# Kernel tuning notes

Measured on AMD Instinct MI355X. Metric: run time of the kernel, lower is better.

## Reference

```python
import jax, jax.numpy as jnp
import numpy as np

B, C_LIDAR, C_CAM = 2, 384, 80
H = W = 180
HW = H * W
HID, NCLS, P, NH, DFF, L, NMS_K = 128, 10, 200, 8, 256, 2, 3


def conv2d(x, w, b):
    y = jax.lax.conv_general_dilated(x, w, (1, 1), 'SAME', dimension_numbers=('NCHW', 'OIHW', 'NCHW'))
    return y + b[None, :, None, None]


def conv1d3(x, w, b):
    y = jax.lax.conv_general_dilated(x, w, (1,), 'SAME', dimension_numbers=('NCH', 'OIH', 'NCH'))
    return y + b[None, :, None]


def layer_norm(x, g, b, eps=1e-5):
    mu = jnp.mean(x, -1, keepdims=True)
    var = jnp.mean((x - mu) ** 2, -1, keepdims=True)
    return (x - mu) * jax.lax.rsqrt(var + eps) * g + b


def mha(q, k, v, wqkv, bqkv, wo, bo):
    Bq, Nq, C = q.shape
    dh = C // NH
    qh = (q @ wqkv[0].T + bqkv[0]).reshape(Bq, Nq, NH, dh)
    kh = (k @ wqkv[1].T + bqkv[1]).reshape(k.shape[0], -1, NH, dh)
    vh = (v @ wqkv[2].T + bqkv[2]).reshape(v.shape[0], -1, NH, dh)
    att = jax.nn.softmax(jnp.einsum('bqhd,bkhd->bhqk', qh, kh) * np.float32(1.0 / np.sqrt(dh)), axis=-1)
    out = jnp.einsum('bhqk,bkhd->bqhd', att, vh).reshape(Bq, Nq, C)
    return out @ wo.T + bo


def posembed(pos, w1, b1, g, bt, w2, b2):
    # Conv1d(2->C,k1) + BN(inference) + ReLU + Conv1d(C->C,k1); pos [B,N,2] -> [B,N,C]
    x = pos @ w1.T + b1
    x = jax.nn.relu(x * g + bt)
    return x @ w2.T + b2


def reference(lidar, cam, shared_w, shared_b, fused_w, fused_b, hm_w1, hm_b1, hm_g, hm_beta, hm_w2, hm_b2, ce_w, ce_b, pe_w1, pe_b1, pe_g, pe_beta, pe_w2, pe_b2, attn_wqkv, attn_bqkv, attn_wo, attn_bo, ln_g, ln_b, ffn_w1, ffn_b1, ffn_w2, ffn_b2, hc_w1, hc_b1, hc_g, hc_beta, hc_w2, hc_b2, hh_w1, hh_b1, hh_g, hh_beta, hh_w2, hh_b2):
    cam_feat = conv2d(cam, fused_w, fused_b)            # [B,HID,H,W]
    lidar_feat = conv2d(lidar, shared_w, shared_b)      # [B,HID,H,W]
    lidar_flat = lidar_feat.reshape(B, HID, HW)
    key_flat = cam_feat.reshape(B, HID, HW).transpose(0, 2, 1)   # [B,HW,HID]
    # heatmap head: ConvModule(conv+BN+ReLU) then conv -> classes
    h = jax.nn.relu(conv2d(lidar_feat, hm_w1, hm_b1) * hm_g[None, :, None, None] + hm_beta[None, :, None, None])
    dense_heatmap = conv2d(h, hm_w2, hm_b2)             # [B,NCLS,H,W]
    heatmap = jax.nn.sigmoid(jax.lax.stop_gradient(dense_heatmap))
    # max-pool local-max NMS
    pad = NMS_K // 2
    inner = jax.lax.reduce_window(heatmap, -jnp.inf, jax.lax.max, (1, 1, NMS_K, NMS_K), (1, 1, 1, 1), 'VALID')
    local_max = jnp.zeros_like(heatmap).at[:, :, pad:-pad, pad:-pad].set(inner)
    # nuScenes: classes 8,9 use kernel-size-1 pooling (identity)
    local_max = local_max.at[:, 8].set(heatmap[:, 8]).at[:, 9].set(heatmap[:, 9])
    heatmap = heatmap * (heatmap == local_max)
    # top-k proposals over flattened class*HW scores (== descending argsort[:P])
    _, top = jax.lax.top_k(heatmap.reshape(B, -1), P)
    top_cls = top // HW
    top_idx = top % HW
    qf = jnp.take_along_axis(lidar_flat, top_idx[:, None, :], axis=2)   # [B,HID,P]
    one_hot = jax.nn.one_hot(top_cls, NCLS, dtype=qf.dtype)             # [B,P,NCLS]
    qf = qf + (one_hot @ ce_w.T + ce_b).transpose(0, 2, 1)
    # BEV position grid (x/y cell centers, ij order matching HW flattening)
    gx = jnp.arange(H, dtype=qf.dtype) + 0.5
    gy = jnp.arange(W, dtype=qf.dtype) + 0.5
    bev = jnp.stack(jnp.meshgrid(gx, gy, indexing='ij'), -1).reshape(HW, 2)
    qpos = bev[top_idx]                                  # [B,P,2]
    x = qf.transpose(0, 2, 1)                            # [B,P,HID]
    for i in range(L):
        qpe = posembed(qpos, pe_w1[i, 0], pe_b1[i, 0], pe_g[i, 0], pe_beta[i, 0], pe_w2[i, 0], pe_b2[i, 0])
        kpe = posembed(bev[None], pe_w1[i, 1], pe_b1[i, 1], pe_g[i, 1], pe_beta[i, 1], pe_w2[i, 1], pe_b2[i, 1])
        k = key_flat + kpe
        sa = mha(x + qpe, x + qpe, x + qpe, attn_wqkv[i, 0], attn_bqkv[i, 0], attn_wo[i, 0], attn_bo[i, 0])
        x = layer_norm(x + sa, ln_g[i, 0], ln_b[i, 0])
        ca = mha(x + qpe, k, k, attn_wqkv[i, 1], attn_bqkv[i, 1], attn_wo[i, 1], attn_bo[i, 1])
        x = layer_norm(x + ca, ln_g[i, 1], ln_b[i, 1])
        f = jax.nn.relu(x @ ffn_w1[i].T + ffn_b1[i]) @ ffn_w2[i].T + ffn_b2[i]
        x = layer_norm(x + f, ln_g[i, 2], ln_b[i, 2])
        xc = x.transpose(0, 2, 1)                        # [B,HID,P]
        yc = jax.nn.relu(conv1d3(xc, hc_w1[i], hc_b1[i]) * hc_g[i][None, :, None] + hc_beta[i][None, :, None])
        center = conv1d3(yc, hc_w2[i], hc_b2[i]) + qpos.transpose(0, 2, 1)
        yh = jax.nn.relu(conv1d3(xc, hh_w1[i], hh_b1[i]) * hh_g[i][None, :, None] + hh_beta[i][None, :, None])
        hm_pred = conv1d3(yh, hh_w2[i], hh_b2[i])
        qpos = jax.lax.stop_gradient(center).transpose(0, 2, 1)   # .detach().clone().permute
    return jnp.concatenate([center, hm_pred], axis=1)   # [B, 2+NCLS, P]


def _n(key, i, shape, s=0.02):
    return s * jax.random.normal(jax.random.fold_in(key, i), shape, dtype=jnp.float32)


def setup_inputs():
    key = jax.random.key(0)
    z, o = jnp.zeros, jnp.ones
    return dict(
        lidar=jax.random.normal(jax.random.fold_in(key, 100), (B, C_LIDAR, H, W), dtype=jnp.float32),
        cam=jax.random.normal(jax.random.fold_in(key, 101), (B, C_CAM, H, W), dtype=jnp.float32),
        shared_w=_n(key, 0, (HID, C_LIDAR, 3, 3)), shared_b=z((HID,)),
        fused_w=_n(key, 1, (HID, C_CAM, 3, 3)), fused_b=z((HID,)),
        hm_w1=_n(key, 2, (HID, HID, 3, 3)), hm_b1=z((HID,)), hm_g=o((HID,)), hm_beta=z((HID,)),
        hm_w2=_n(key, 3, (NCLS, HID, 3, 3)), hm_b2=z((NCLS,)),
        ce_w=_n(key, 4, (HID, NCLS)), ce_b=z((HID,)),
        pe_w1=_n(key, 5, (L, 2, HID, 2), 0.1), pe_b1=z((L, 2, HID)),
        pe_g=o((L, 2, HID)), pe_beta=z((L, 2, HID)),
        pe_w2=_n(key, 6, (L, 2, HID, HID)), pe_b2=z((L, 2, HID)),
        attn_wqkv=_n(key, 7, (L, 2, 3, HID, HID), 0.05), attn_bqkv=z((L, 2, 3, HID)),
        attn_wo=_n(key, 8, (L, 2, HID, HID), 0.05), attn_bo=z((L, 2, HID)),
        ln_g=o((L, 3, HID)), ln_b=z((L, 3, HID)),
        ffn_w1=_n(key, 9, (L, DFF, HID)), ffn_b1=z((L, DFF)),
        ffn_w2=_n(key, 10, (L, HID, DFF)), ffn_b2=z((L, HID)),
        hc_w1=_n(key, 11, (L, HID, HID, 3)), hc_b1=z((L, HID)), hc_g=o((L, HID)), hc_beta=z((L, HID)),
        hc_w2=_n(key, 12, (L, 2, HID, 3)), hc_b2=z((L, 2)),
        hh_w1=_n(key, 13, (L, HID, HID, 3)), hh_b1=z((L, HID)), hh_g=o((L, HID)), hh_beta=z((L, HID)),
        hh_w2=_n(key, 14, (L, NCLS, HID, 3)), hh_b2=z((L, NCLS)),
    )
```

## Files before the change

### kernel.cpp

```cpp
#include <hip/hip_runtime.h>
#include <hip/hip_bf16.h>

typedef __hip_bfloat16 bf16;
typedef _Float16 f16;

#define HW 32400
#define NCLS 10
#define PQ 200
#define HIDDEN 128
#define NSPLIT 45
#define SPLITLEN 720
#define QT 100
#define CAP 6144
#define NBIN 4096

typedef __attribute__((ext_vector_type(8))) _Float16 half8;
typedef __attribute__((ext_vector_type(8))) short short8;
typedef __attribute__((ext_vector_type(4))) short short4v;
typedef __attribute__((ext_vector_type(4))) float f32x4;

__device__ __forceinline__ float b2f(bf16 v) { return __bfloat162float(v); }
__device__ __forceinline__ void stf(float* p, float v) { *p = v; }
__device__ __forceinline__ void stf(bf16* p, float v) { *p = __float2bfloat16(v); }
__device__ __forceinline__ float ldsel(const void* p, long i, unsigned isbf) {
  return isbf ? __bfloat162float(((const bf16*)p)[i]) : ((const float*)p)[i];
}
__device__ __forceinline__ float ldf(const float* p, long i) { return p[i]; }
__device__ __forceinline__ float ldf(const bf16* p, long i) { return __bfloat162float(p[i]); }
__device__ __forceinline__ short f2bf_bits(float v) {
  union { bf16 h; short s; } u; u.h = __float2bfloat16(v); return u.s;
}
__device__ __forceinline__ short f2h_bits(float v) {
  union { f16 h; short s; } u; u.h = (f16)v; return u.s;
}

__global__ void detect_k(const unsigned* __restrict__ L, unsigned* __restrict__ FLAGS)
{
  __shared__ unsigned cnt[2];
  int tid = threadIdx.x;
  if (tid < 2) cnt[tid] = 0;
  __syncthreads();
  unsigned nz = 0, pl = 0;
  for (int w = tid; w < 4096; w += 256) {
    unsigned u = L[w];
    if (u) {
      nz++;
      unsigned e = (u >> 7) & 0xFF;
      if (e >= 110 && e <= 140) pl++;
    }
  }
  atomicAdd(&cnt[0], nz);
  atomicAdd(&cnt[1], pl);
  __syncthreads();
  if (tid == 0) {
    FLAGS[0] = (2u * cnt[1] > cnt[0]) ? 1u : 0u;
    FLAGS[1] = 0u;
  }
}

struct CvtArgs { const void* src[40]; int n[40]; int off[40]; };
__global__ __launch_bounds__(256) void cvt_k(CvtArgs a, float* __restrict__ dst,
                                             const unsigned* __restrict__ FLAGS)
{
  int j = blockIdx.y;
  unsigned isbf = FLAGS[0];
  int n = a.n[j];
  const void* s = a.src[j];
  float* d = dst + a.off[j];
  for (int t = blockIdx.x * 256 + threadIdx.x; t < n; t += gridDim.x * 256)
    d[t] = ldsel(s, t, isbf);
}

__global__ __launch_bounds__(256) void wprep_k(const float* __restrict__ Wsrc,
    short* __restrict__ WB, int N, int K, int KB, int NTG, int split,
    const unsigned* __restrict__ FLAGS, int dynmode)
{
  unsigned isbf = dynmode ? FLAGS[0] : 0u;
  long total = (long)(split ? 2 : 1) * 9 * KB * NTG * 512;
  for (long t = (long)blockIdx.x * 256 + threadIdx.x; t < total;
       t += (long)gridDim.x * 256) {
    long r = t;
    int k = (int)(r & 31); r >>= 5;
    int n16 = (int)(r & 15); r >>= 4;
    int nt = (int)(r % NTG); r /= NTG;
    int kb = (int)(r % KB); r /= KB;
    int tap = (int)(r % 9); r /= 9;
    int plane = (int)r;
    int n = nt * 16 + n16, kk = kb * 32 + k;
    float v = 0.f;
    if (n < N && kk < K) v = Wsrc[((long)n * K + kk) * 9 + tap];
    short outv;
    if (isbf) {
      outv = (plane == 0) ? f2bf_bits(v) : (short)0;
    } else {
      f16 h = (f16)v;
      if (plane == 0) outv = f2h_bits((float)h);
      else outv = f2h_bits((v - (float)h) * 4096.0f);
    }
    WB[t] = outv;
  }
}

template <int MODE, int WM, int WN, int MT, int NT, typename CT>
__global__ __launch_bounds__(256) void conv_mfma(
    const void* __restrict__ A, const unsigned* __restrict__ FLAGS, int dyn,
    int gate, long abatch,
    const short* __restrict__ WB, const float* __restrict__ bias,
    const float* __restrict__ g, const float* __restrict__ beta, int act,
    CT* __restrict__ C, long cbatch, int N, int K, int KB, int NTG)
{
  constexpr int AW = 3 * 66 * 40;
  __shared__ __align__(16) short Ah[AW];
  __shared__ __align__(16) short Al[MODE == 3 ? AW : 8];
  if (gate >= 0 && FLAGS[0] != (unsigned)gate) return;
  int gsw = blockIdx.x;
  int idx = (gsw & 7) * 68 + (gsw >> 3);
  if (idx >= 540) return;
  unsigned isbf = dyn ? FLAGS[0] : 0u;
  int bz = blockIdx.z;
  int y = idx / 3;
  int x0 = (idx % 3) * 60;
  int tid = threadIdx.x;
  int w = tid >> 6, lane = tid & 63;
  int lane15 = lane & 15, lgrp = lane >> 4;
  int wm = w % WM, wn = w / WM;
  int mbase = wm * MT * 16;
  int nbase = wn * NT * 16;
  f32x4 accM[MT][NT] = {};
  f32x4 accC[MODE == 3 ? MT : 1][MODE == 3 ? NT : 1] = {};
  long planeStride = (long)9 * KB * NTG * 512;

  for (int kb = 0; kb < KB; kb++) {
    __syncthreads();
    for (int u = tid; u < 3 * 66 * 4; u += 256) {
      int px = u % 66;
      int t2 = u / 66;
      int kg = t2 & 3, row = t2 >> 2;
      int gx = x0 + px - 1, gy = y + row - 1;
      bool in = (gx >= 0 && gx < 180 && gy >= 0 && gy < 180);
      long gbase = (long)bz * abatch + (long)(kb * 32 + kg * 8) * HW +
                   (long)gy * 180 + gx;
      short8 hv, lv;
#pragma unroll
      for (int j = 0; j < 8; j++) {
        int kk = kb * 32 + kg * 8 + j;
        float v = (in && kk < K) ? ldsel(A, gbase + (long)j * HW, isbf) : 0.f;
        if constexpr (MODE == 1) {
          hv[j] = f2bf_bits(v);
        } else {
          f16 h = (f16)v;
          hv[j] = f2h_bits((float)h);
          if constexpr (MODE == 3) lv[j] = f2h_bits((v - (float)h) * 4096.0f);
        }
      }
      int o = (row * 66 + px) * 40 + kg * 8;
      *(short8*)&Ah[o] = hv;
      if constexpr (MODE == 3) *(short8*)&Al[o] = lv;
    }
    __syncthreads();
#pragma unroll
    for (int tap = 0; tap < 9; tap++) {
      int ty = tap / 3, tx = tap % 3;
      const short* wb = WB + (((long)tap * KB + kb) * NTG) * 512;
      if constexpr (MODE == 1) {
        short8 bh[NT];
#pragma unroll
        for (int nt = 0; nt < NT; nt++) {
          long o = (long)(wn * NT + nt) * 512 + lane15 * 32 + lgrp * 8;
          bh[nt] = *(const short8*)(wb + o);
        }
        short8 ah[MT];
#pragma unroll
        for (int mt = 0; mt < MT; mt++) {
          int px = mbase + mt * 16 + lane15 + tx;
          ah[mt] = *(const short8*)&Ah[(ty * 66 + px) * 40 + lgrp * 8];
        }
#pragma unroll
        for (int mt = 0; mt < MT; mt++)
#pragma unroll
          for (int nt = 0; nt < NT; nt++)
            accM[mt][nt] = __builtin_amdgcn_mfma_f32_16x16x32_bf16(
                ah[mt], bh[nt], accM[mt][nt], 0, 0, 0);
      } else {
        half8 bh[NT], bl[MODE == 3 ? NT : 1];
#pragma unroll
        for (int nt = 0; nt < NT; nt++) {
          long o = (long)(wn * NT + nt) * 512 + lane15 * 32 + lgrp * 8;
          bh[nt] = *(const half8*)(wb + o);
          if constexpr (MODE == 3) bl[nt] = *(const half8*)(wb + planeStride + o);
        }
        half8 ah[MT], al[MODE == 3 ? MT : 1];
#pragma unroll
        for (int mt = 0; mt < MT; mt++) {
          int px = mbase + mt * 16 + lane15 + tx;
          int o = (ty * 66 + px) * 40 + lgrp * 8;
          ah[mt] = *(const half8*)&Ah[o];
          if constexpr (MODE == 3) al[mt] = *(const half8*)&Al[o];
        }
#pragma unroll
        for (int mt = 0; mt < MT; mt++)
#pragma unroll
          for (int nt = 0; nt < NT; nt++) {
            accM[mt][nt] = __builtin_amdgcn_mfma_f32_16x16x32_f16(
                ah[mt], bh[nt], accM[mt][nt], 0, 0, 0);
            if constexpr (MODE == 3) {
              accC[mt][nt] = __builtin_amdgcn_mfma_f32_16x16x32_f16(
                  al[mt], bh[nt], accC[mt][nt], 0, 0, 0);
              accC[mt][nt] = __builtin_amdgcn_mfma_f32_16x16x32_f16(
                  ah[mt], bl[nt], accC[mt][nt], 0, 0, 0);
            }
          }
      }
    }
  }
  int pixbase = y * 180 + x0;
#pragma unroll
  for (int mt = 0; mt < MT; mt++) {
    int m = mbase + mt * 16 + lgrp * 4;
    if (m >= 60) continue;
#pragma unroll
    for (int nt = 0; nt < NT; nt++) {
      int n = nbase + nt * 16 + lane15;
      if (n >= N) continue;
      float bi = bias[n];
      float gg = g ? g[n] : 1.f;
      float bb = g ? beta[n] : 0.f;
      long base = (long)bz * cbatch + (long)n * HW + pixbase + m;
      if constexpr (sizeof(CT) == 4) {
        f32x4 ov;
#pragma unroll
        for (int r = 0; r < 4; r++) {
          float v = accM[mt][nt][r];
          if constexpr (MODE == 3) v += accC[mt][nt][r] * (1.f / 4096.f);
          v += bi;
          if (g) v = v * gg + bb;
          if (act == 1) v = fmaxf(v, 0.f);
          else if (act == 2) v = 1.f / (1.f + expf(-v));
          ov[r] = v;
        }
        *(f32x4*)&C[base] = ov;
      } else {
        short4v ov;
#pragma unroll
        for (int r = 0; r < 4; r++) {
          float v = accM[mt][nt][r];
          if constexpr (MODE == 3) v += accC[mt][nt][r] * (1.f / 4096.f);
          v += bi;
          if (g) v = v * gg + bb;
          if (act == 1) v = fmaxf(v, 0.f);
          ov[r] = f2bf_bits(v);
        }
        *(short4v*)&C[base] = ov;
      }
    }
  }
}

__global__ __launch_bounds__(256) void kvproj_k(
    const bf16* __restrict__ A1, const bf16* __restrict__ A2,
    const float* __restrict__ Wf, const float* __restrict__ bias,
    bf16* __restrict__ C)
{
  __shared__ __align__(16) short As[64 * 40];
  int m0 = blockIdx.x * 64;
  int n0 = blockIdx.y * 64;
  int b = blockIdx.z;
  int tid = threadIdx.x;
  int w = tid >> 6, lane = tid & 63;
  int lane15 = lane & 15, lgrp = lane >> 4;
  int wm = w & 1, wn = w >> 1;
  const bf16* A1b = A1 + (long)b * 128 * HW;
  f32x4 acc[2][2] = {};
  for (int kb = 0; kb < 4; kb++) {
    __syncthreads();
    for (int e = tid; e < 2048; e += 256) {
      int k = e >> 6, m = e & 63;
      int gm = m0 + m;
      float v = 0.f;
      if (gm < HW) {
        long idx = (long)(kb * 32 + k) * HW + gm;
        v = b2f(A1b[idx]) + b2f(A2[idx]);
      }
      As[m * 40 + k] = f2bf_bits(v);
    }
    __syncthreads();
    short8 bh[2];
#pragma unroll
    for (int nt = 0; nt < 2; nt++) {
      int n = n0 + wn * 32 + nt * 16 + lane15;
      const float* wr = Wf + (long)n * 128 + kb * 32 + lgrp * 8;
      float4 w0 = *(const float4*)wr;
      float4 w1 = *(const float4*)(wr + 4);
      short8 t;
      t[0] = f2bf_bits(w0.x); t[1] = f2bf_bits(w0.y);
      t[2] = f2bf_bits(w0.z); t[3] = f2bf_bits(w0.w);
      t[4] = f2bf_bits(w1.x); t[5] = f2bf_bits(w1.y);
      t[6] = f2bf_bits(w1.z); t[7] = f2bf_bits(w1.w);
      bh[nt] = t;
    }
    short8 ah[2];
#pragma unroll
    for (int mt = 0; mt < 2; mt++) {
      int m = wm * 32 + mt * 16 + lane15;
      ah[mt] = *(const short8*)&As[m * 40 + lgrp * 8];
    }
#pragma unroll
    for (int mt = 0; mt < 2; mt++)
#pragma unroll
      for (int nt = 0; nt < 2; nt++)
        acc[mt][nt] = __builtin_amdgcn_mfma_f32_16x16x32_bf16(
            ah[mt], bh[nt], acc[mt][nt], 0, 0, 0);
  }
#pragma unroll
  for (int mt = 0; mt < 2; mt++) {
    int mq = m0 + wm * 32 + mt * 16 + lgrp * 4;
    if (mq >= HW) continue;
#pragma unroll
    for (int nt = 0; nt < 2; nt++) {
      int n = n0 + wn * 32 + nt * 16 + lane15;
      float bi = bias[n];
      short4v ov;
#pragma unroll
      for (int r = 0; r < 4; r++) ov[r] = f2bf_bits(acc[mt][nt][r] + bi);
      *(short4v*)&C[(long)b * 256 * HW + (long)n * HW + mq] = ov;
    }
  }
}

template <typename AT, typename CT>
__global__ __launch_bounds__(256) void gemm_k(
    const AT* __restrict__ A, const AT* __restrict__ A2, int lda, int amode,
    long abatch,
    const float* __restrict__ W, const float* __restrict__ bias, int act,
    const float* __restrict__ res,
    const float* __restrict__ pe1w, const float* __restrict__ pe1b,
    const float* __restrict__ pe1g, const float* __restrict__ pe1bt,
    CT* __restrict__ C, int ldc, int cmode, long cbatch,
    int M, int N, int K)
{
  __shared__ __align__(16) float As[16][68];
  __shared__ __align__(16) float Ws[16][68];
  int b = blockIdx.z;
  int m0 = blockIdx.x * 64, n0 = blockIdx.y * 64;
  int tid = threadIdx.x;
  int nt = tid & 15, mt = tid >> 4;
  float acc[4][4] = {};
  const AT* Ab = A + (long)b * abatch;
  for (int k0 = 0; k0 < K; k0 += 16) {
    if (amode == 0) {
      for (int e = tid; e < 1024; e += 256) {
        int m = e >> 4, k = e & 15;
        float v = 0.f;
        if (m0 + m < M) {
          long idx = (long)(m0 + m) * lda + k0 + k;
          v = ldf(Ab, idx);
          if (A2) v += ldf(A2, idx);
        }
        As[k][m] = v;
      }
    } else if (amode == 2) {
      for (int e = tid; e < 1024; e += 256) {
        int m = e & 63, k = e >> 6;
        float v = 0.f;
        int gm = m0 + m;
        if (gm < M) {
          float p0 = (float)(gm / 180) + 0.5f;
          float p1 = (float)(gm % 180) + 0.5f;
          int kk = k0 + k;
          float t = p0 * pe1w[kk * 2] + p1 * pe1w[kk * 2 + 1] + pe1b[kk];
          t = t * pe1g[kk] + pe1bt[kk];
          v = fmaxf(t, 0.f);
        }
        As[k][m] = v;
      }
    } else {
      const float* qp = (const float*)A;
      for (int e = tid; e < 1024; e += 256) {
        int m = e & 63, k = e >> 6;
        float v = 0.f;
        int gm = m0 + m;
        if (gm < M) {
          float p0 = qp[gm * 2], p1 = qp[gm * 2 + 1];
          int kk = k0 + k;
          float t = p0 * pe1w[kk * 2] + p1 * pe1w[kk * 2 + 1] + pe1b[kk];
          t = t * pe1g[kk] + pe1bt[kk];
          v = fmaxf(t, 0.f);
        }
        As[k][m] = v;
      }
    }
    for (int e = tid; e < 1024; e += 256) {
      int n = e >> 4, k = e & 15;
      float v = 0.f;
      if (n0 + n < N) v = W[(long)(n0 + n) * K + k0 + k];
      Ws[k][n] = v;
    }
    __syncthreads();
#pragma unroll
    for (int kk = 0; kk < 16; kk++) {
      float4 av = *(const float4*)&As[kk][mt * 4];
      float4 wv = *(const float4*)&Ws[kk][nt * 4];
      float am[4] = {av.x, av.y, av.z, av.w};
      float wn[4] = {wv.x, wv.y, wv.z, wv.w};
#pragma unroll
      for (int mi = 0; mi < 4; mi++)
#pragma unroll
        for (int ni = 0; ni < 4; ni++)
          acc[mi][ni] = fmaf(am[mi], wn[ni], acc[mi][ni]);
    }
    __syncthreads();
  }
#pragma unroll
  for (int mi = 0; mi < 4; mi++) {
    int m = m0 + mt * 4 + mi;
    if (m >= M) continue;
#pragma unroll
    for (int ni = 0; ni < 4; ni++) {
      int n = n0 + nt * 4 + ni;
      if (n >= N) continue;
      float v = acc[mi][ni];
      if (bias) v += bias[n];
      if (act == 1) v = fmaxf(v, 0.f);
      if (res) v += res[(long)m * ldc + n];
      long ci = (cmode == 0) ? ((long)b * cbatch + (long)m * ldc + n)
                             : ((long)b * cbatch + (long)n * ldc + m);
      stf(&C[ci], v);
    }
  }
}

__global__ void nms_k(const float* __restrict__ HEAT, float* __restrict__ SCORE)
{
  int t = blockIdx.x * 256 + threadIdx.x;
  if (t >= 2 * NCLS * HW) return;
  int b = t / (NCLS * HW); int r = t % (NCLS * HW);
  int cls = r / HW; int n = r % HW;
  const float* hb = HEAT + ((long)(b * NCLS + cls)) * HW;
  float v = hb[n];
  bool keep = true;
  if (cls < 8) {
    int y = n / 180, x = n % 180;
    if (y == 0 || y == 179 || x == 0 || x == 179) keep = false;
    else {
      float mx = -1e30f;
#pragma unroll
      for (int dy = -1; dy <= 1; dy++)
#pragma unroll
        for (int dx = -1; dx <= 1; dx++)
          mx = fmaxf(mx, hb[(y + dy) * 180 + x + dx]);
      keep = (v == mx);
    }
  }
  SCORE[(long)b * (NCLS * HW) + r] = keep ? v : 0.f;
}

__global__ void zero_u32(unsigned* p, int n)
{
  int t = blockIdx.x * 256 + threadIdx.x;
  if (t < n) p[t] = 0;
}

__global__ __launch_bounds__(256) void hist_k(const float* __restrict__ SCORE,
                                              unsigned* __restrict__ HIST)
{
  __shared__ unsigned lh[NBIN];
  int b = blockIdx.y;
  for (int e = threadIdx.x; e < NBIN; e += 256) lh[e] = 0;
  __syncthreads();
  int start = blockIdx.x * 1350;
  const float* sb = SCORE + (long)b * (NCLS * HW);
  for (int e = start + threadIdx.x; e < start + 1350; e += 256) {
    unsigned bits = __float_as_uint(sb[e]);
    atomicAdd(&lh[bits >> 18], 1u);
  }
  __syncthreads();
  for (int e = threadIdx.x; e < NBIN; e += 256) {
    unsigned c = lh[e];
    if (c) atomicAdd(&HIST[b * NBIN + e], c);
  }
}

__global__ void thresh_k(const unsigned* __restrict__ HIST, unsigned* __restrict__ THR)
{
  __shared__ unsigned ps[256];
  int b = blockIdx.x;
  const unsigned* hb = HIST + b * NBIN;
  unsigned s = 0;
  for (int j = 0; j < 16; j++) s += hb[threadIdx.x * 16 + j];
  ps[threadIdx.x] = s;
  __syncthreads();
  if (threadIdx.x == 0) {
    unsigned cum = 0; int t = 255;
    for (; t > 0; t--) { if (cum + ps[t] >= PQ) break; cum += ps[t]; }
    int bin = t * 16 + 15;
    for (; bin > t * 16; bin--) { unsigned c = hb[bin]; if (cum + c >= PQ) break; cum += c; }
    if (bin < 1) bin = 1;
    THR[b] = (unsigned)bin;
  }
}

__global__ void collect_k(const float* __restrict__ SCORE, const unsigned* __restrict__ THR,
                          unsigned* __restrict__ ACNT, unsigned long long* __restrict__ CAND)
{
  int t = blockIdx.x * 256 + threadIdx.x;
  if (t >= 2 * NCLS * HW) return;
  int b = t / (NCLS * HW); int r = t % (NCLS * HW);
  float v = SCORE[(long)b * (NCLS * HW) + r];
  unsigned bits = __float_as_uint(v);
  if ((bits >> 18) >= THR[b]) {
    unsigned slot = atomicAdd(&ACNT[b], 1u);
    if (slot < CAP) CAND[(long)b * CAP + slot] =
        ((unsigned long long)bits << 32) | (unsigned)(~r);
  }
}

__global__ __launch_bounds__(64) void select_k(
    const unsigned long long* __restrict__ CAND, const unsigned* __restrict__ ACNT,
    unsigned* __restrict__ TOPC, unsigned* __restrict__ TOPI, float* __restrict__ QPA)
{
  __shared__ unsigned long long cnd[CAP];
  int b = blockIdx.x;
  int lane = threadIdx.x;
  unsigned cnt = ACNT[b]; if (cnt > CAP) cnt = CAP;
  for (int e = lane; e < (int)cnt; e += 64) cnd[e] = CAND[(long)b * CAP + e];
  __syncthreads();
  for (int p = 0; p < PQ; p++) {
    unsigned long long best = 0;
    for (int e = lane; e < (int)cnt; e += 64) { unsigned long long c = cnd[e]; if (c > best) best = c; }
#pragma unroll
    for (int o = 32; o; o >>= 1) {
      unsigned long long other = __shfl_xor(best, o, 64);
      if (other > best) best = other;
    }
    for (int e = lane; e < (int)cnt; e += 64) if (best != 0 && cnd[e] == best) cnd[e] = 0;
    if (lane == 0) {
      unsigned idx = (best == 0) ? 0u : ~(unsigned)(best & 0xFFFFFFFFull);
      if (idx >= NCLS * HW) idx = 0;
      unsigned cls = idx / HW, n = idx % HW;
      TOPC[b * PQ + p] = cls; TOPI[b * PQ + p] = n;
      QPA[((long)(b * PQ + p)) * 2 + 0] = (float)(n / 180) + 0.5f;
      QPA[((long)(b * PQ + p)) * 2 + 1] = (float)(n % 180) + 0.5f;
    }
    __syncthreads();
  }
}

__global__ void gather_k(const float* __restrict__ LIDF, const unsigned* __restrict__ TOPC,
                         const unsigned* __restrict__ TOPI, const float* __restrict__ cew,
                         const float* __restrict__ ceb, float* __restrict__ X)
{
  int t = blockIdx.x * 256 + threadIdx.x;
  if (t >= 2 * PQ * HIDDEN) return;
  int c = t & 127; int r = t >> 7; int p = r % PQ; int b = r / PQ;
  unsigned n = TOPI[b * PQ + p]; unsigned cls = TOPC[b * PQ + p];
  if (n >= HW) n = 0;
  if (cls >= NCLS) cls = 0;
  X[t] = LIDF[((long)(b * HIDDEN + c)) * HW + n] + cew[c * NCLS + cls] + ceb[c];
}

__global__ __launch_bounds__(64) void self_attn_k(const float* __restrict__ SQKV,
                                                  float* __restrict__ SAO)
{
  int q = blockIdx.x, h = blockIdx.y, b = blockIdx.z;
  int lane = threadIdx.x;
  const float* qp = SQKV + ((long)(b * PQ + q)) * 384 + h * 16;
  float qv[16];
#pragma unroll
  for (int d = 0; d < 16; d++) qv[d] = qp[d] * 0.25f;
  float sv[4]; int kks[4]; int nk = 0;
  float lmax = -1e30f;
  for (int kk = lane; kk < PQ; kk += 64) {
    const float* kp = SQKV + ((long)(b * PQ + kk)) * 384 + 128 + h * 16;
    float s = 0.f;
#pragma unroll
    for (int d = 0; d < 16; d++) s = fmaf(qv[d], kp[d], s);
    sv[nk] = s; kks[nk] = kk; nk++;
    lmax = fmaxf(lmax, s);
  }
#pragma unroll
  for (int o = 32; o; o >>= 1) lmax = fmaxf(lmax, __shfl_xor(lmax, o, 64));
  float lsum = 0.f; float acc[16] = {};
  for (int t = 0; t < nk; t++) {
    float p = expf(sv[t] - lmax);
    lsum += p;
    const float* vp = SQKV + ((long)(b * PQ + kks[t])) * 384 + 256 + h * 16;
#pragma unroll
    for (int d = 0; d < 16; d++) acc[d] = fmaf(p, vp[d], acc[d]);
  }
#pragma unroll
  for (int o = 32; o; o >>= 1) lsum += __shfl_xor(lsum, o, 64);
#pragma unroll
  for (int d = 0; d < 16; d++) {
    float v = acc[d];
#pragma unroll
    for (int o = 32; o; o >>= 1) v += __shfl_xor(v, o, 64);
    if (lane == 0) SAO[((long)(b * PQ + q)) * HIDDEN + h * 16 + d] = v / lsum;
  }
}

__global__ __launch_bounds__(256) void flash_k(const float* __restrict__ QH,
                                               const bf16* __restrict__ KVT,
                                               float* __restrict__ PART)
{
  int s = blockIdx.x, h = blockIdx.y;
  int b = blockIdx.z >> 1, qh = blockIdx.z & 1;
  int tid = threadIdx.x;
  __shared__ __align__(16) float sL[QT][36];
  __shared__ __align__(16) float qtL[16][104];
  __shared__ __align__(16) float kjL[2][16][36];
  __shared__ __align__(16) float vjL[2][16][36];
  __shared__ float mL[QT], lL[QT], aL[QT];
  int qbase = qh * QT;
  for (int e = tid; e < QT * 16; e += 256) {
    int q = e >> 4, d = e & 15;
    qtL[d][q] = QH[((long)(b * PQ + qbase + q)) * HIDDEN + h * 16 + d] * 0.25f;
  }
  if (tid < QT) { mL[tid] = -1e30f; lL[tid] = 0.f; }
  float ovr[4][2] = {};
  int qg = tid >> 3, jg = tid & 7;
  int q0 = qg * 4, j0 = jg * 4;
  int pd = (tid & 7) * 2;
  int nbeg = s * SPLITLEN;
  const bf16* Kb = KVT + (long)b * 256 * HW + (long)(h * 16) * HW;
  const bf16* Vb = Kb + (long)128 * HW;
  int sd = tid >> 4, sj = (tid & 15) * 2;
  {
    long o = (long)sd * HW + nbeg + sj;
    float2 kv, vv;
    kv.x = b2f(Kb[o]);     kv.y = b2f(Kb[o + 1]);
    vv.x = b2f(Vb[o]);     vv.y = b2f(Vb[o + 1]);
    *(float2*)&kjL[0][sd][sj] = kv;
    *(float2*)&vjL[0][sd][sj] = vv;
  }
  __syncthreads();
  const int ntiles = (SPLITLEN + 31) / 32;
  for (int t = 0; t < ntiles; t++) {
    int cur = t & 1;
    if (t + 1 < ntiles) {
      int n0 = nbeg + (t + 1) * 32;
      int rem = SPLITLEN - (t + 1) * 32; if (rem > 32) rem = 32;
      float2 kv = {0.f, 0.f}, vv = {0.f, 0.f};
      if (sj < rem) {
        long o = (long)sd * HW + n0 + sj;
        kv.x = b2f(Kb[o]); vv.x = b2f(Vb[o]);
        if (sj + 1 < rem) { kv.y = b2f(Kb[o + 1]); vv.y = b2f(Vb[o + 1]); }
      }
      *(float2*)&kjL[cur ^ 1][sd][sj] = kv;
      *(float2*)&vjL[cur ^ 1][sd][sj] = vv;
    }
    int remt = SPLITLEN - t * 32; if (remt > 32) remt = 32;
    if (tid < 200) {
      float acc[4][4] = {};
#pragma unroll
      for (int d = 0; d < 16; d++) {
        float4 kv = *(const float4*)&kjL[cur][d][j0];
        float4 qv = *(const float4*)&qtL[d][q0];
        float qa[4] = {qv.x, qv.y, qv.z, qv.w};
        float ka[4] = {kv.x, kv.y, kv.z, kv.w};
#pragma unroll
        for (int i = 0; i < 4; i++)
#pragma unroll
          for (int jj = 0; jj < 4; jj++)
            acc[i][jj] = fmaf(qa[i], ka[jj], acc[i][jj]);
      }
      if (remt < 32) {
#pragma unroll
        for (int i = 0; i < 4; i++)
#pragma unroll
          for (int jj = 0; jj < 4; jj++)
            if (j0 + jj >= remt) acc[i][jj] = -1e30f;
      }
#pragma unroll
      for (int i = 0; i < 4; i++) {
        float mx = fmaxf(fmaxf(acc[i][0], acc[i][1]), fmaxf(acc[i][2], acc[i][3]));
        mx = fmaxf(mx, __shfl_xor(mx, 1, 64));
        mx = fmaxf(mx, __shfl_xor(mx, 2, 64));
        mx = fmaxf(mx, __shfl_xor(mx, 4, 64));
        float mold = mL[q0 + i];
        float mnew = fmaxf(mx, mold);
        float ls = 0.f;
#pragma unroll
        for (int jj = 0; jj < 4; jj++) {
          float p = expf(acc[i][jj] - mnew);
          acc[i][jj] = p;
          ls += p;
        }
        ls += __shfl_xor(ls, 1, 64);
        ls += __shfl_xor(ls, 2, 64);
        ls += __shfl_xor(ls, 4, 64);
        if (jg == 0) {
          float al = expf(mold - mnew);
          lL[q0 + i] = lL[q0 + i] * al + ls;
          mL[q0 + i] = mnew;
          aL[q0 + i] = al;
        }
        float4 ov;
        ov.x = acc[i][0]; ov.y = acc[i][1]; ov.z = acc[i][2]; ov.w = acc[i][3];
        *(float4*)&sL[q0 + i][j0] = ov;
      }
    }
    __syncthreads();
    if (tid < 200) {
#pragma unroll
      for (int i = 0; i < 4; i++) {
        float a = aL[qg + 25 * i];
        ovr[i][0] *= a; ovr[i][1] *= a;
      }
#pragma unroll
      for (int j00 = 0; j00 < 32; j00 += 4) {
        float4 v0 = *(const float4*)&vjL[cur][pd][j00];
        float4 v1 = *(const float4*)&vjL[cur][pd + 1][j00];
#pragma unroll
        for (int i = 0; i < 4; i++) {
          float4 p = *(const float4*)&sL[qg + 25 * i][j00];
          ovr[i][0] = fmaf(p.x, v0.x, ovr[i][0]);
          ovr[i][0] = fmaf(p.y, v0.y, ovr[i][0]);
          ovr[i][0] = fmaf(p.z, v0.z, ovr[i][0]);
          ovr[i][0] = fmaf(p.w, v0.w, ovr[i][0]);
          ovr[i][1] = fmaf(p.x, v1.x, ovr[i][1]);
          ovr[i][1] = fmaf(p.y, v1.y, ovr[i][1]);
          ovr[i][1] = fmaf(p.z, v1.z, ovr[i][1]);
          ovr[i][1] = fmaf(p.w, v1.w, ovr[i][1]);
        }
      }
    }
    __syncthreads();
  }
  long base = ((((long)(b * 8 + h)) * NSPLIT + s) * PQ) * 18;
  if (tid < 200) {
#pragma unroll
    for (int i = 0; i < 4; i++) {
      long ro = base + (long)(qbase + qg + 25 * i) * 18;
      PART[ro + pd] = ovr[i][0];
      PART[ro + pd + 1] = ovr[i][1];
    }
  }
  if (tid < QT) {
    long ro = base + (long)(qbase + tid) * 18;
    PART[ro + 16] = mL[tid];
    PART[ro + 17] = lL[tid];
  }
}

__global__ void combine_k(const float* __restrict__ PART, float* __restrict__ CAO)
{
  int t = blockIdx.x * 256 + threadIdx.x;
  if (t >= 2 * 8 * PQ * 16) return;
  int d = t & 15; int r = t >> 4;
  int q = r % PQ; r /= PQ;
  int h = r & 7; int b = r >> 3;
  long base = (((long)(b * 8 + h)) * NSPLIT) * PQ * 18 + (long)q * 18;
  float M = -1e30f;
  for (int s = 0; s < NSPLIT; s++) M = fmaxf(M, PART[base + (long)s * PQ * 18 + 16]);
  float L = 0.f, O = 0.f;
  for (int s = 0; s < NSPLIT; s++) {
    long p0 = base + (long)s * PQ * 18;
    float w = expf(PART[p0 + 16] - M);
    L += PART[p0 + 17] * w;
    O += PART[p0 + d] * w;
  }
  CAO[((long)(b * PQ + q)) * HIDDEN + h * 16 + d] = (L > 0.f) ? O / L : 0.f;
}

__global__ __launch_bounds__(256) void ln_k(const float* __restrict__ PRE,
                                            const float* __restrict__ g,
                                            const float* __restrict__ bta,
                                            float* __restrict__ X)
{
  int row = blockIdx.x * 4 + (threadIdx.x >> 6);
  int lane = threadIdx.x & 63;
  const float* p = PRE + (long)row * HIDDEN;
  float v0 = p[lane], v1 = p[lane + 64];
  float s = v0 + v1;
#pragma unroll
  for (int o = 32; o; o >>= 1) s += __shfl_xor(s, o, 64);
  float mu = s * (1.f / 128.f);
  float d0 = v0 - mu, d1 = v1 - mu;
  float vs = d0 * d0 + d1 * d1;
#pragma unroll
  for (int o = 32; o; o >>= 1) vs += __shfl_xor(vs, o, 64);
  float rs = rsqrtf(vs * (1.f / 128.f) + 1e-5f);
  float* xo = X + (long)row * HIDDEN;
  xo[lane] = d0 * rs * g[lane] + bta[lane];
  xo[lane + 64] = d1 * rs * g[lane + 64] + bta[lane + 64];
}

__global__ __launch_bounds__(128) void conv1d_k(const float* __restrict__ X,
                                                const float* __restrict__ w,
                                                const float* __restrict__ bias,
                                                const float* __restrict__ g,
                                                const float* __restrict__ beta,
                                                float* __restrict__ Y)
{
  int p = blockIdx.x, b = blockIdx.y;
  int co = threadIdx.x;
  __shared__ float xs[3][HIDDEN];
  for (int e = co; e < 3 * HIDDEN; e += HIDDEN) {
    int t = e >> 7, c = e & 127;
    int pp = p + t - 1;
    xs[t][c] = (pp >= 0 && pp < PQ) ? X[((long)(b * PQ + pp)) * HIDDEN + c] : 0.f;
  }
  __syncthreads();
  const float* wr = w + (long)co * HIDDEN * 3;
  float acc = 0.f;
  for (int c = 0; c < HIDDEN; c++) {
    acc = fmaf(xs[0][c], wr[c * 3 + 0], acc);
    acc = fmaf(xs[1][c], wr[c * 3 + 1], acc);
    acc = fmaf(xs[2][c], wr[c * 3 + 2], acc);
  }
  float v = (acc + bias[co]) * g[co] + beta[co];
  Y[((long)(b * PQ + p)) * HIDDEN + co] = fmaxf(v, 0.f);
}

__global__ void head2_k(const float* __restrict__ Y, const float* __restrict__ w,
                        const float* __restrict__ bias, const float* __restrict__ qpos,
                        float* __restrict__ OUT, int N, float* __restrict__ qnext)
{
  int t = blockIdx.x * 256 + threadIdx.x;
  if (t >= 2 * N * PQ) return;
  int p = t % PQ; int r = t / PQ; int co = r % N; int b = r / N;
  const float* wr = w + (long)co * HIDDEN * 3;
  float acc = 0.f;
  for (int tap = 0; tap < 3; tap++) {
    int pp = p + tap - 1;
    if (pp < 0 || pp >= PQ) continue;
    const float* yr = Y + ((long)(b * PQ + pp)) * HIDDEN;
    for (int c = 0; c < HIDDEN; c++)
      acc = fmaf(yr[c], wr[c * 3 + tap], acc);
  }
  float v = acc + bias[co];
  if (qpos) v += qpos[((long)(b * PQ + p)) * 2 + co];
  OUT[((long)(b * N + co)) * PQ + p] = v;
  if (qnext) qnext[((long)(b * PQ + p)) * 2 + co] = v;
}

__global__ void out_k(const float* __restrict__ CENT, const float* __restrict__ HMP,
                      void* __restrict__ out, const unsigned* __restrict__ FLAGS)
{
  int t = blockIdx.x * 256 + threadIdx.x;
  if (t >= 2 * 12 * PQ) return;
  int p = t % PQ; int r = t / PQ; int ch = r % 12; int b = r / 12;
  float v = (ch < 2) ? CENT[((long)(b * 2 + ch)) * PQ + p]
                     : HMP[((long)(b * 10 + ch - 2)) * PQ + p];
  if (FLAGS[0]) ((bf16*)out)[t] = __float2bfloat16(v);
  else          ((float*)out)[t] = v;
}

extern "C" void kernel_launch(void* const* d_in, const int* in_sizes, int n_in,
                              void* d_out, int out_size, void* d_ws, size_t ws_size,
                              hipStream_t stream)
{
  (void)n_in; (void)out_size; (void)ws_size;

  float* F = (float*)d_ws;
  size_t off = 0;
  int aoff[42];
  {
    size_t acc = 0;
    for (int i = 2; i < 42; i++) { aoff[i] = (int)acc; acc += (size_t)in_sizes[i]; }
    off = acc;
  }
  float* ARENA = F;
  float* LIDF = F + off;
  bf16*  KVT16 = (bf16*)(F + off);
  off += 8294400;
  float* HBUF = F + off;
  bf16*  KPET16 = (bf16*)(F + off);
  float* PART  = F + off;
  off += 4147200;
  bf16*  CAMF16 = (bf16*)(F + off);
  off += 4147200;
  float* HEAT  = F + off;
  float* SCORE = F + off + 648000;
  off += 1296000;
  float* X   = F + off; off += 51200;
  float* XQ  = F + off; off += 51200;
  float* QPE = F + off; off += 51200;
  float* T1Q = F + off; off += 51200;
  float* SQKV = F + off; off += 153600;
  float* SAO = F + off; off += 51200;
  float* PRE = F + off; off += 51200;
  float* QH2 = F + off; off += 51200;
  float* CAO = F + off; off += 51200;
  float* FF1 = F + off; off += 102400;
  float* YC  = F + off; off += 51200;
  float* CENT = F + off; off += 800;
  float* HMP = F + off; off += 4000;
  float* QPA = F + off; off += 800;
  float* QPB = F + off; off += 800;
  unsigned* U = (unsigned*)(F + off);
  unsigned* HIST  = U;
  unsigned* ACNT  = U + 8192;
  unsigned* THR   = U + 8194;
  unsigned* FLAGS = U + 8196;
  unsigned* TOPC  = U + 8198;
  unsigned* TOPI  = U + 8598;
  unsigned long long* CAND = (unsigned long long*)(U + 9000);
  short* WB_LID = (short*)((((uintptr_t)X) + 15) & ~(uintptr_t)15);
  short* WB_CAM = WB_LID + 884736;
  short* WB_HM1 = WB_CAM + 110592;
  short* WB_HM2 = WB_HM1 + 294912;

  auto W = [&](int i) -> const float* { return ARENA + aoff[i]; };

  detect_k<<<1, 256, 0, stream>>>((const unsigned*)d_in[0], FLAGS);
  {
    CvtArgs a;
    for (int i = 2; i < 42; i++) { a.src[i - 2] = d_in[i]; a.n[i - 2] = in_sizes[i]; a.off[i - 2] = aoff[i]; }
    cvt_k<<<dim3(432, 40), 256, 0, stream>>>(a, ARENA, FLAGS);
  }
  wprep_k<<<3456, 256, 0, stream>>>(W(2), WB_LID, 128, 384, 12, 8, 1, FLAGS, 1);
  wprep_k<<<432, 256, 0, stream>>>(W(4), WB_CAM, 128, 80, 3, 8, 0, FLAGS, 1);
  wprep_k<<<1152, 256, 0, stream>>>(W(6), WB_HM1, 128, 128, 4, 8, 1, FLAGS, 0);
  wprep_k<<<144, 256, 0, stream>>>(W(10), WB_HM2, 10, 128, 4, 1, 1, FLAGS, 0);

  auto gemm = [&](const float* A, const float* A2, int lda, const float* Wp,
                  const float* bias, int act, const float* res, float* C, int ldc,
                  int M, int N, int K) {
    dim3 grid((M + 63) / 64, (N + 63) / 64, 1);
    gemm_k<float, float><<<grid, 256, 0, stream>>>(
        A, A2, lda, 0, 0L, Wp, bias, act, res,
        nullptr, nullptr, nullptr, nullptr, C, ldc, 0, 0L, M, N, K);
  };

  conv_mfma<1, 1, 4, 4, 2, float><<<dim3(544, 1, 2), 256, 0, stream>>>(
      d_in[0], FLAGS, 1, 1, (long)384 * HW, WB_LID, W(3), nullptr, nullptr, 0,
      LIDF, (long)128 * HW, 128, 384, 12, 8);
  conv_mfma<3, 1, 4, 4, 2, float><<<dim3(544, 1, 2), 256, 0, stream>>>(
      d_in[0], FLAGS, 1, 0, (long)384 * HW, WB_LID, W(3), nullptr, nullptr, 0,
      LIDF, (long)128 * HW, 128, 384, 12, 8);
  conv_mfma<1, 1, 4, 4, 2, bf16><<<dim3(544, 1, 2), 256, 0, stream>>>(
      d_in[1], FLAGS, 1, 1, (long)80 * HW, WB_CAM, W(5), nullptr, nullptr, 0,
      CAMF16, (long)128 * HW, 128, 80, 3, 8);
  conv_mfma<0, 1, 4, 4, 2, bf16><<<dim3(544, 1, 2), 256, 0, stream>>>(
      d_in[1], FLAGS, 1, 0, (long)80 * HW, WB_CAM, W(5), nullptr, nullptr, 0,
      CAMF16, (long)128 * HW, 128, 80, 3, 8);
  for (int b = 0; b < 2; b++) {
    conv_mfma<3, 1, 4, 4, 2, float><<<dim3(544, 1, 1), 256, 0, stream>>>(
        LIDF + (long)b * 128 * HW, FLAGS, 0, -1, 0L, WB_HM1, W(7), W(8), W(9), 1,
        HBUF, 0L, 128, 128, 4, 8);
    conv_mfma<3, 4, 1, 1, 1, float><<<dim3(544, 1, 1), 256, 0, stream>>>(
        HBUF, FLAGS, 0, -1, 0L, WB_HM2, W(11), nullptr, nullptr, 2,
        HEAT + (long)b * NCLS * HW, 0L, 10, 128, 4, 1);
  }

  nms_k<<<(2 * NCLS * HW + 255) / 256, 256, 0, stream>>>(HEAT, SCORE);
  zero_u32<<<(8196 + 255) / 256, 256, 0, stream>>>(U, 8196);
  hist_k<<<dim3(240, 2), 256, 0, stream>>>(SCORE, HIST);
  thresh_k<<<2, 256, 0, stream>>>(HIST, THR);
  collect_k<<<(2 * NCLS * HW + 255) / 256, 256, 0, stream>>>(SCORE, THR, ACNT, CAND);
  select_k<<<2, 64, 0, stream>>>(CAND, ACNT, TOPC, TOPI, QPA);
  gather_k<<<200, 256, 0, stream>>>(LIDF, TOPC, TOPI, W(12), W(13), X);

  for (int i = 0; i < 2; i++) {
    const float* qcur = (i == 0) ? QPA : QPB;
    float* qnext = (i == 0) ? QPB : QPA;
    gemm_k<float, float><<<dim3(7, 2, 1), 256, 0, stream>>>(
        qcur, (const float*)nullptr, 0, 3, 0L,
        W(18) + (size_t)(i * 2 + 0) * 16384, W(19) + (i * 2 + 0) * 128, 0, nullptr,
        W(14) + (i * 2 + 0) * 256, W(15) + (i * 2 + 0) * 128,
        W(16) + (i * 2 + 0) * 128, W(17) + (i * 2 + 0) * 128,
        QPE, 128, 0, 0L, 400, 128, 128);
    gemm_k<float, bf16><<<dim3(507, 2, 1), 256, 0, stream>>>(
        ARENA, (const float*)nullptr, 0, 2, 0L,
        W(18) + (size_t)(i * 2 + 1) * 16384, W(19) + (i * 2 + 1) * 128, 0, nullptr,
        W(14) + (i * 2 + 1) * 256, W(15) + (i * 2 + 1) * 128,
        W(16) + (i * 2 + 1) * 128, W(17) + (i * 2 + 1) * 128,
        KPET16, HW, 1, 0L, 32400, 128, 128);
    gemm(X, QPE, 128, W(20) + (size_t)(i * 2 + 0) * 49152, W(21) + (i * 2 + 0) * 384,
         0, nullptr, SQKV, 384, 400, 384, 128);
    self_attn_k<<<dim3(200, 8, 2), 64, 0, stream>>>(SQKV, SAO);
    gemm(SAO, nullptr, 128, W(22) + (size_t)(i * 2 + 0) * 16384, W(23) + (i * 2 + 0) * 128,
         0, X, PRE, 128, 400, 128, 128);
    ln_k<<<100, 256, 0, stream>>>(PRE, W(24) + (i * 3 + 0) * 128, W(25) + (i * 3 + 0) * 128, X);
    gemm(X, QPE, 128, W(20) + (size_t)(i * 2 + 1) * 49152, W(21) + (i * 2 + 1) * 384,
         0, nullptr, QH2, 128, 400, 384, 128);
    kvproj_k<<<dim3(507, 4, 2), 256, 0, stream>>>(
        CAMF16, KPET16,
        W(20) + (size_t)(i * 2 + 1) * 49152 + 16384,
        W(21) + (i * 2 + 1) * 384 + 128, KVT16);
    flash_k<<<dim3(NSPLIT, 8, 4), 256, 0, stream>>>(QH2, KVT16, PART);
    combine_k<<<200, 256, 0, stream>>>(PART, CAO);
    gemm(CAO, nullptr, 128, W(22) + (size_t)(i * 2 + 1) * 16384, W(23) + (i * 2 + 1) * 128,
         0, X, PRE, 128, 400, 128, 128);
    ln_k<<<100, 256, 0, stream>>>(PRE, W(24) + (i * 3 + 1) * 128, W(25) + (i * 3 + 1) * 128, X);
    gemm(X, nullptr, 128, W(26) + (size_t)i * 32768, W(27) + i * 256,
         1, nullptr, FF1, 256, 400, 256, 128);
    gemm(FF1, nullptr, 256, W(28) + (size_t)i * 32768, W(29) + i * 128,
         0, X, PRE, 128, 400, 128, 256);
    ln_k<<<100, 256, 0, stream>>>(PRE, W(24) + (i * 3 + 2) * 128, W(25) + (i * 3 + 2) * 128, X);
    conv1d_k<<<dim3(200, 2), 128, 0, stream>>>(X, W(30) + (size_t)i * 49152,
        W(31) + i * 128, W(32) + i * 128, W(33) + i * 128, YC);
    head2_k<<<4, 256, 0, stream>>>(YC, W(34) + (size_t)i * 768, W(35) + i * 2,
        qcur, CENT, 2, qnext);
    conv1d_k<<<dim3(200, 2), 128, 0, stream>>>(X, W(36) + (size_t)i * 49152,
        W(37) + i * 128, W(38) + i * 128, W(39) + i * 128, YC);
    head2_k<<<16, 256, 0, stream>>>(YC, W(40) + (size_t)i * 3840, W(41) + i * 10,
        nullptr, HMP, 10, nullptr);
  }
  out_k<<<19, 256, 0, stream>>>(CENT, HMP, d_out, FLAGS);
}
```

Before: 2.149 ms.

## Rewrite cross-attention flash kernel to use bf16 MFMA for QK and PV

```diff
diff --git a/kernel.cpp b/kernel.cpp
--- a/kernel.cpp
+++ b/kernel.cpp
@@ -10,9 +10,10 @@
 #define HIDDEN 128
 #define NSPLIT 45
 #define SPLITLEN 720
-#define QT 100
+#define CHK 32
 #define CAP 6144
 #define NBIN 4096
+#define L2E 1.44269504f
 
 typedef __attribute__((ext_vector_type(8))) _Float16 half8;
 typedef __attribute__((ext_vector_type(8))) short short8;
@@ -598,147 +599,108 @@
   }
 }
 
-__global__ __launch_bounds__(256) void flash_k(const float* __restrict__ QH,
-                                               const bf16* __restrict__ KVT,
-                                               float* __restrict__ PART)
-{
+__global__ __launch_bounds__(256) void flash_mfma_k(const float* __restrict__ QH,
+                                                    const bf16* __restrict__ KVT,
+                                                    float* __restrict__ PART)
+{
+  __shared__ __align__(16) short Qs[64 * 40];
+  __shared__ __align__(16) short Ks[2][32 * 40];
+  __shared__ __align__(16) short Vs[2][16 * 40];
+  __shared__ __align__(16) short Ps[4][16 * 40];
   int s = blockIdx.x, h = blockIdx.y;
-  int b = blockIdx.z >> 1, qh = blockIdx.z & 1;
+  int b = blockIdx.z >> 2, qb = blockIdx.z & 3;
   int tid = threadIdx.x;
-  __shared__ __align__(16) float sL[QT][36];
-  __shared__ __align__(16) float qtL[16][104];
-  __shared__ __align__(16) float kjL[2][16][36];
-  __shared__ __align__(16) float vjL[2][16][36];
-  __shared__ float mL[QT], lL[QT], aL[QT];
-  int qbase = qh * QT;
-  for (int e = tid; e < QT * 16; e += 256) {
-    int q = e >> 4, d = e & 15;
-    qtL[d][q] = QH[((long)(b * PQ + qbase + q)) * HIDDEN + h * 16 + d] * 0.25f;
-  }
-  if (tid < QT) { mL[tid] = -1e30f; lL[tid] = 0.f; }
-  float ovr[4][2] = {};
-  int qg = tid >> 3, jg = tid & 7;
-  int q0 = qg * 4, j0 = jg * 4;
-  int pd = (tid & 7) * 2;
+  int w = tid >> 6, lane = tid & 63;
+  int lane15 = lane & 15, lgrp = lane >> 4;
+  const short* Kb = (const short*)KVT + ((long)b * 256 + h * 16) * HW;
+  const short* Vb = Kb + (long)128 * HW;
   int nbeg = s * SPLITLEN;
-  const bf16* Kb = KVT + (long)b * 256 * HW + (long)(h * 16) * HW;
-  const bf16* Vb = Kb + (long)128 * HW;
-  int sd = tid >> 4, sj = (tid & 15) * 2;
+
+  for (int e = tid; e < 2 * 32 * 16; e += 256) {
+    int buf = e >> 9, rr = e & 511;
+    int kk = rr >> 4, d2 = rr & 15;
+    Ks[buf][kk * 40 + 16 + d2] = 0;
+  }
   {
-    long o = (long)sd * HW + nbeg + sj;
-    float2 kv, vv;
-    kv.x = b2f(Kb[o]);     kv.y = b2f(Kb[o + 1]);
-    vv.x = b2f(Vb[o]);     vv.y = b2f(Vb[o + 1]);
-    *(float2*)&kjL[0][sd][sj] = kv;
-    *(float2*)&vjL[0][sd][sj] = vv;
-  }
+    int q = tid >> 2, dg = tid & 3;
+    int gq = qb * 64 + q;
+    short8 v = {};
+    if (dg < 2 && gq < PQ) {
+      const float* qp = QH + ((long)(b * PQ + gq)) * HIDDEN + h * 16 + dg * 8;
+#pragma unroll
+      for (int j = 0; j < 8; j++) v[j] = f2bf_bits(qp[j] * 0.25f);
+    }
+    *(short8*)&Qs[q * 40 + dg * 8] = v;
+  }
+
+  auto stageKV = [&](int t, int buf) {
+    int kb0 = nbeg + t * CHK;
+    for (int e = tid; e < 512; e += 256) {
+      int d = e >> 5, kk = e & 31;
+      long gk = kb0 + kk; if (gk >= HW) gk = HW - 1;
+      long go = (long)d * HW + gk;
+      Ks[buf][kk * 40 + d] = Kb[go];
+      Vs[buf][d * 40 + kk] = Vb[go];
+    }
+  };
+
+  stageKV(0, 0);
   __syncthreads();
-  const int ntiles = (SPLITLEN + 31) / 32;
-  for (int t = 0; t < ntiles; t++) {
+
+  short8 aq = *(const short8*)&Qs[(w * 16 + lane15) * 40 + lgrp * 8];
+  float m[4] = {-1e30f, -1e30f, -1e30f, -1e30f};
+  float l[4] = {0.f, 0.f, 0.f, 0.f};
+  f32x4 accO = {};
+  const int NTL = (SPLITLEN + CHK - 1) / CHK;
+  for (int t = 0; t < NTL; t++) {
     int cur = t & 1;
-    if (t + 1 < ntiles) {
-      int n0 = nbeg + (t + 1) * 32;
-      int rem = SPLITLEN - (t + 1) * 32; if (rem > 32) rem = 32;
-      float2 kv = {0.f, 0.f}, vv = {0.f, 0.f};
-      if (sj < rem) {
-        long o = (long)sd * HW + n0 + sj;
-        kv.x = b2f(Kb[o]); vv.x = b2f(Vb[o]);
-        if (sj + 1 < rem) { kv.y = b2f(Kb[o + 1]); vv.y = b2f(Vb[o + 1]); }
-      }
-      *(float2*)&kjL[cur ^ 1][sd][sj] = kv;
-      *(float2*)&vjL[cur ^ 1][sd][sj] = vv;
-    }
-    int remt = SPLITLEN - t * 32; if (remt > 32) remt = 32;
-    if (tid < 200) {
-      float acc[4][4] = {};
-#pragma unroll
-      for (int d = 0; d < 16; d++) {
-        float4 kv = *(const float4*)&kjL[cur][d][j0];
-        float4 qv = *(const float4*)&qtL[d][q0];
-        float qa[4] = {qv.x, qv.y, qv.z, qv.w};
-        float ka[4] = {kv.x, kv.y, kv.z, kv.w};
-#pragma unroll
-        for (int i = 0; i < 4; i++)
-#pragma unroll
-          for (int jj = 0; jj < 4; jj++)
-            acc[i][jj] = fmaf(qa[i], ka[jj], acc[i][jj]);
-      }
-      if (remt < 32) {
-#pragma unroll
-        for (int i = 0; i < 4; i++)
-#pragma unroll
-          for (int jj = 0; jj < 4; jj++)
-            if (j0 + jj >= remt) acc[i][jj] = -1e30f;
-      }
-#pragma unroll
-      for (int i = 0; i < 4; i++) {
-        float mx = fmaxf(fmaxf(acc[i][0], acc[i][1]), fmaxf(acc[i][2], acc[i][3]));
-        mx = fmaxf(mx, __shfl_xor(mx, 1, 64));
-        mx = fmaxf(mx, __shfl_xor(mx, 2, 64));
-        mx = fmaxf(mx, __shfl_xor(mx, 4, 64));
-        float mold = mL[q0 + i];
-        float mnew = fmaxf(mx, mold);
-        float ls = 0.f;
-#pragma unroll
-        for (int jj = 0; jj < 4; jj++) {
-          float p = expf(acc[i][jj] - mnew);
-          acc[i][jj] = p;
-          ls += p;
-        }
-        ls += __shfl_xor(ls, 1, 64);
-        ls += __shfl_xor(ls, 2, 64);
-        ls += __shfl_xor(ls, 4, 64);
-        if (jg == 0) {
-          float al = expf(mold - mnew);
-          lL[q0 + i] = lL[q0 + i] * al + ls;
-          mL[q0 + i] = mnew;
-          aL[q0 + i] = al;
-        }
-        float4 ov;
-        ov.x = acc[i][0]; ov.y = acc[i][1]; ov.z = acc[i][2]; ov.w = acc[i][3];
-        *(float4*)&sL[q0 + i][j0] = ov;
-      }
-    }
+    if (t + 1 < NTL) stageKV(t + 1, cur ^ 1);
+    int valid = SPLITLEN - t * CHK; if (valid > CHK) valid = CHK;
+    short8 bk0 = *(const short8*)&Ks[cur][lane15 * 40 + lgrp * 8];
+    short8 bk1 = *(const short8*)&Ks[cur][(16 + lane15) * 40 + lgrp * 8];
+    f32x4 z = {};
+    f32x4 s0 = __builtin_amdgcn_mfma_f32_16x16x32_bf16(aq, bk0, z, 0, 0, 0);
+    f32x4 s1 = __builtin_amdgcn_mfma_f32_16x16x32_bf16(aq, bk1, z, 0, 0, 0);
+    bool msk0 = (lane15 >= valid);
+    bool msk1 = (16 + lane15 >= valid);
+#pragma unroll
+    for (int r = 0; r < 4; r++) {
+      float x0 = msk0 ? -1e30f : s0[r];
+      float x1 = msk1 ? -1e30f : s1[r];
+      float mx = fmaxf(x0, x1);
+      mx = fmaxf(mx, __shfl_xor(mx, 1, 64));
+      mx = fmaxf(mx, __shfl_xor(mx, 2, 64));
+      mx = fmaxf(mx, __shfl_xor(mx, 4, 64));
+      mx = fmaxf(mx, __shfl_xor(mx, 8, 64));
+      float mn = fmaxf(m[r], mx);
+      float p0 = exp2f((x0 - mn) * L2E);
+      float p1 = exp2f((x1 - mn) * L2E);
+      float sum = p0 + p1;
+      sum += __shfl_xor(sum, 1, 64);
+      sum += __shfl_xor(sum, 2, 64);
+      sum += __shfl_xor(sum, 4, 64);
+      sum += __shfl_xor(sum, 8, 64);
+      float al = exp2f((m[r] - mn) * L2E);
+      l[r] = l[r] * al + sum;
+      m[r] = mn;
+      accO[r] *= al;
+      Ps[w][(lgrp * 4 + r) * 40 + lane15] = f2bf_bits(p0);
+      Ps[w][(lgrp * 4 + r) * 40 + 16 + lane15] = f2bf_bits(p1);
+    }
+    short8 ap = *(const short8*)&Ps[w][lane15 * 40 + lgrp * 8];
+    short8 bv = *(const short8*)&Vs[cur][lane15 * 40 + lgrp * 8];
+    accO = __builtin_amdgcn_mfma_f32_16x16x32_bf16(ap, bv, accO, 0, 0, 0);
     __syncthreads();
-    if (tid < 200) {
-#pragma unroll
-      for (int i = 0; i < 4; i++) {
-        float a = aL[qg + 25 * i];
-        ovr[i][0] *= a; ovr[i][1] *= a;
-      }
-#pragma unroll
-      for (int j00 = 0; j00 < 32; j00 += 4) {
-        float4 v0 = *(const float4*)&vjL[cur][pd][j00];
-        float4 v1 = *(const float4*)&vjL[cur][pd + 1][j00];
-#pragma unroll
-        for (int i = 0; i < 4; i++) {
-          float4 p = *(const float4*)&sL[qg + 25 * i][j00];
-          ovr[i][0] = fmaf(p.x, v0.x, ovr[i][0]);
-          ovr[i][0] = fmaf(p.y, v0.y, ovr[i][0]);
-          ovr[i][0] = fmaf(p.z, v0.z, ovr[i][0]);
-          ovr[i][0] = fmaf(p.w, v0.w, ovr[i][0]);
-          ovr[i][1] = fmaf(p.x, v1.x, ovr[i][1]);
-          ovr[i][1] = fmaf(p.y, v1.y, ovr[i][1]);
-          ovr[i][1] = fmaf(p.z, v1.z, ovr[i][1]);
-          ovr[i][1] = fmaf(p.w, v1.w, ovr[i][1]);
-        }
-      }
-    }
-    __syncthreads();
   }
   long base = ((((long)(b * 8 + h)) * NSPLIT + s) * PQ) * 18;
-  if (tid < 200) {
-#pragma unroll
-    for (int i = 0; i < 4; i++) {
-      long ro = base + (long)(qbase + qg + 25 * i) * 18;
-      PART[ro + pd] = ovr[i][0];
-      PART[ro + pd + 1] = ovr[i][1];
-    }
-  }
-  if (tid < QT) {
-    long ro = base + (long)(qbase + tid) * 18;
-    PART[ro + 16] = mL[tid];
-    PART[ro + 17] = lL[tid];
+#pragma unroll
+  for (int r = 0; r < 4; r++) {
+    int gq = qb * 64 + w * 16 + lgrp * 4 + r;
+    if (gq < PQ) {
+      long ro = base + (long)gq * 18;
+      PART[ro + lane15] = accO[r];
+      if (lane15 == 0) { PART[ro + 16] = m[r]; PART[ro + 17] = l[r]; }
+    }
   }
 }
 
@@ -974,12 +936,12 @@
          0, X, PRE, 128, 400, 128, 128);
     ln_k<<<100, 256, 0, stream>>>(PRE, W(24) + (i * 3 + 0) * 128, W(25) + (i * 3 + 0) * 128, X);
     gemm(X, QPE, 128, W(20) + (size_t)(i * 2 + 1) * 49152, W(21) + (i * 2 + 1) * 384,
-         0, nullptr, QH2, 128, 400, 384, 128);
+         0, nullptr, QH2, 128, 400, 128, 128);
     kvproj_k<<<dim3(507, 4, 2), 256, 0, stream>>>(
         CAMF16, KPET16,
         W(20) + (size_t)(i * 2 + 1) * 49152 + 16384,
         W(21) + (i * 2 + 1) * 384 + 128, KVT16);
-    flash_k<<<dim3(NSPLIT, 8, 4), 256, 0, stream>>>(QH2, KVT16, PART);
+    flash_mfma_k<<<dim3(NSPLIT, 8, 8), 256, 0, stream>>>(QH2, KVT16, PART);
     combine_k<<<200, 256, 0, stream>>>(PART, CAO);
     gemm(CAO, nullptr, 128, W(22) + (size_t)(i * 2 + 1) * 16384, W(23) + (i * 2 + 1) * 128,
          0, X, PRE, 128, 400, 128, 128);
```

Result: faster. 1.962 ms (-8.7%).
